# Kernel optimization log

Hardware: AMD Instinct MI355X
Metric: run time of the kernel (lower is better)

Reference implementation:

```python
import jax, jax.numpy as jnp
import numpy as np

C = 96          # channels (= output_dim)
NUM_HEADS = 6
DILS = (1, 2, 3)
KS_ATT = 3      # dilate-attention kernel size
KS_COR = 5      # self-correlation kernel size
PAD_COR = 2
LN_EPS = 1e-5


def _unfold(x, k, dil, pad):
    # torch.nn.Unfold(kernel=k, dilation=dil, padding=pad, stride=1)
    # x: [B, C, H, W] -> [B, C, k*k, H, W] (channel-major, kernel row-major)
    B, c, H, W = x.shape
    xp = jnp.pad(x, ((0, 0), (0, 0), (pad, pad), (pad, pad)))
    patches = [xp[:, :, i * dil:i * dil + H, j * dil:j * dil + W]
               for i in range(k) for j in range(k)]
    return jnp.stack(patches, axis=2)


def _layernorm(x, g, b):
    m = jnp.mean(x, axis=-1, keepdims=True)
    v = jnp.mean((x - m) ** 2, axis=-1, keepdims=True)
    return (x - m) * jax.lax.rsqrt(v + LN_EPS) * g + b


def _dilate_attn(q, k, v, dil, head_dim, scale):
    # q,k,v: [B, cb, H, W] with cb = C // num_dilation
    B, cb, H, W = q.shape
    heads = cb // head_dim
    qf = q.reshape(B, heads, head_dim, H * W)                                  # bhdn
    kp = _unfold(k, KS_ATT, dil, dil).reshape(B, heads, head_dim, KS_ATT * KS_ATT, H * W)
    attn = jax.nn.softmax(jnp.einsum('bhdn,bhdkn->bhnk', qf, kp) * scale, axis=-1)
    vp = _unfold(v, KS_ATT, dil, dil).reshape(B, heads, head_dim, KS_ATT * KS_ATT, H * W)
    out = jnp.einsum('bhnk,bhdkn->bnhd', attn, vp)                             # [B,HW,heads,hd]
    return out.reshape(B, H, W, cb)


def _forward(x, g1, b1, Wqkv, bqkv, Wproj, bproj, g2, b2, W1, bm1, W2, bm2):
    B, Cc, H, W = x.shape
    nd = len(DILS)
    head_dim = Cc // NUM_HEADS
    scale = head_dim ** (-0.5)

    xh = jnp.transpose(x, (0, 2, 3, 1))                                        # [B,H,W,C]

    # --- MultiDilatelocalAttention block ---
    y = _layernorm(xh, g1, b1)
    qkv = jnp.einsum('bhwc,oc->bhwo', y, Wqkv) + bqkv                          # 1x1 conv == linear
    qkv = jnp.transpose(qkv, (0, 3, 1, 2)).reshape(B, 3, nd, Cc // nd, H, W)
    outs = []
    for i, d in enumerate(DILS):
        outs.append(_dilate_attn(qkv[:, 0, i], qkv[:, 1, i], qkv[:, 2, i], d, head_dim, scale))
    a = jnp.concatenate(outs, axis=-1)                                         # dilation-major channels
    a = a @ Wproj.T + bproj
    xh = xh + a

    # --- MLP block ---
    z = _layernorm(xh, g2, b2)
    z = jax.nn.gelu(z @ W1.T + bm1, approximate=False) @ W2.T + bm2
    xh = xh + z

    # --- self-correlation ---
    xc = jnp.transpose(xh, (0, 3, 1, 2))                                       # [B,C,H,W]
    xc = jax.nn.relu(xc)
    nrm = jnp.sqrt(jnp.sum(xc * xc, axis=1, keepdims=True))
    xc = xc / jnp.maximum(nrm, 1e-12)                                          # F.normalize dim=1
    pat = _unfold(xc, KS_COR, 1, PAD_COR)                                      # [B,C,25,H,W]
    out = pat.reshape(B, Cc, KS_COR, KS_COR, H, W) * xc[:, :, None, None]
    return jnp.transpose(out, (0, 1, 4, 5, 2, 3))                              # [B,C,H,W,5,5]


def setup_inputs() -> dict:
    key = jax.random.key(0)
    ks = jax.random.split(key, 8)
    B, H, W = 8, 64, 64
    s = 0.02
    return {
        'x': jax.random.normal(ks[0], (B, C, H, W), jnp.float32),
        'g1': jnp.ones((C,), jnp.float32),
        'b1': jnp.zeros((C,), jnp.float32),
        'Wqkv': jax.random.normal(ks[1], (3 * C, C), jnp.float32) * s,
        'bqkv': jnp.zeros((3 * C,), jnp.float32),
        'Wproj': jax.random.normal(ks[2], (C, C), jnp.float32) * s,
        'bproj': jnp.zeros((C,), jnp.float32),
        'g2': jnp.ones((C,), jnp.float32),
        'b2': jnp.zeros((C,), jnp.float32),
        'W1': jax.random.normal(ks[3], (4 * C, C), jnp.float32) * s,
        'bm1': jnp.zeros((4 * C,), jnp.float32),
        'W2': jax.random.normal(ks[4], (C, 4 * C), jnp.float32) * s,
        'bm2': jnp.zeros((C,), jnp.float32),
    }


def reference(x, g1, b1, Wqkv, bqkv, Wproj, bproj, g2, b2, W1, bm1, W2, bm2):
    return _forward(x, g1, b1, Wqkv, bqkv, Wproj, bproj, g2, b2, W1, bm1, W2, bm2)
```

## Files before the change

### kernel.cpp

```cpp
#include <hip/hip_runtime.h>
#include <math.h>

#define NN 4096
#define BN 32768

using short8 = __attribute__((ext_vector_type(8))) short;
using f32x4  = __attribute__((ext_vector_type(4))) float;
typedef unsigned short ushort_t;

__device__ inline unsigned f2bfu(float f) {
    unsigned u = __builtin_bit_cast(unsigned, f);
    u += 0x7FFFu + ((u >> 16) & 1u);
    return u >> 16;
}
__device__ inline ushort_t f2bf(float f) { return (ushort_t)f2bfu(f); }
__device__ inline unsigned pack2(float a, float b) { return f2bfu(a) | (f2bfu(b) << 16); }
__device__ inline float bflo(unsigned u) { return __builtin_bit_cast(float, u << 16); }
__device__ inline float bfhi(unsigned u) { return __builtin_bit_cast(float, u & 0xFFFF0000u); }

__global__ __launch_bounds__(256) void k1_ln_kv(
    const float* __restrict__ x, const float* __restrict__ g1, const float* __restrict__ b1,
    const float* __restrict__ Wqkv, const float* __restrict__ bqkv,
    unsigned* __restrict__ kvt32)
{
    __shared__ __align__(16) float    Cs[96 * 69];
    __shared__ __align__(16) ushort_t As[64 * 104];
    __shared__ __align__(16) ushort_t Bs[96 * 104];
    const int tid = threadIdx.x;
    const long bn0 = (long)blockIdx.x * 64;
    const int b = (int)(bn0 >> 12);
    const int n0 = (int)(bn0 & 4095);

    for (int i = 0; i < 24; ++i) {
        int idx = i * 256 + tid;
        int c = idx >> 6, p = idx & 63;
        Cs[c * 69 + p] = x[((long)(b * 96 + c) << 12) + n0 + p];
    }
    __syncthreads();
    {
        int p = tid >> 2, part = tid & 3, c0 = part * 24;
        float s = 0.f, ss = 0.f;
        for (int c = c0; c < c0 + 24; ++c) { float v = Cs[c*69 + p]; s += v; ss += v*v; }
        s  += __shfl_xor(s, 1);  s  += __shfl_xor(s, 2);
        ss += __shfl_xor(ss, 1); ss += __shfl_xor(ss, 2);
        float m = s * (1.f/96.f);
        float rstd = rsqrtf(ss * (1.f/96.f) - m*m + 1e-5f);
        for (int c = c0; c < c0 + 24; ++c)
            Cs[c*69 + p] = (Cs[c*69 + p] - m) * rstd * g1[c] + b1[c];
    }
    __syncthreads();
    for (int i = 0; i < 12; ++i) {
        int idx = i * 256 + tid;
        int p = idx / 48, cp = idx % 48;
        *(unsigned*)&As[p * 104 + 2*cp] = pack2(Cs[(2*cp)*69 + p], Cs[(2*cp+1)*69 + p]);
    }

    const int lane = tid & 63, wv = tid >> 6;
    const int ln = lane & 15, qd = lane >> 4;
    for (int kv = 0; kv < 2; ++kv) {
        __syncthreads();
        for (int i = 0; i < 9; ++i) {
            int idx = i * 256 + tid;
            int o = idx / 24, q4 = idx % 24;
            float4 wvv = *(const float4*)&Wqkv[(long)(96 + kv*96 + o)*96 + q4*4];
            uint2 d; d.x = pack2(wvv.x, wvv.y); d.y = pack2(wvv.z, wvv.w);
            *(uint2*)&Bs[o * 104 + q4*4] = d;
        }
        __syncthreads();
        f32x4 acc[6];
        #pragma unroll
        for (int t = 0; t < 6; ++t) acc[t] = (f32x4){0.f, 0.f, 0.f, 0.f};
        #pragma unroll
        for (int kc = 0; kc < 3; ++kc) {
            short8 a = *(const short8*)&As[(wv*16 + ln)*104 + kc*32 + qd*8];
            #pragma unroll
            for (int t = 0; t < 6; ++t) {
                short8 bf = *(const short8*)&Bs[(t*16 + ln)*104 + kc*32 + qd*8];
                acc[t] = __builtin_amdgcn_mfma_f32_16x16x32_bf16(a, bf, acc[t], 0, 0, 0);
            }
        }
        #pragma unroll
        for (int t = 0; t < 6; ++t)
            #pragma unroll
            for (int r = 0; r < 4; ++r)
                Cs[(t*16 + ln)*69 + (wv*16 + qd*4 + r)] = acc[t][r];
        __syncthreads();
        for (int i = 0; i < 12; ++i) {
            int idx = i * 256 + tid;
            int cp = idx / 64, p = idx % 64;
            int c = 2*cp;
            unsigned d = pack2(Cs[c*69 + p] + bqkv[96 + kv*96 + c],
                               Cs[(c+1)*69 + p] + bqkv[96 + kv*96 + c + 1]);
            kvt32[((long)(b*96 + kv*48 + cp) << 12) + n0 + p] = d;
        }
    }
}

__global__ __launch_bounds__(256) void k2345(
    const unsigned* __restrict__ kvt32, const float* __restrict__ x,
    const float* __restrict__ g1, const float* __restrict__ b1,
    const float* __restrict__ Wqkv, const float* __restrict__ bqkv,
    const float* __restrict__ Wproj, const float* __restrict__ bproj,
    const float* __restrict__ g2, const float* __restrict__ b2,
    const float* __restrict__ W1, const float* __restrict__ bm1,
    const float* __restrict__ W2, const float* __restrict__ bm2,
    float* __restrict__ xcn)
{
    __shared__ __align__(16) float    Cs[96 * 69];
    __shared__ __align__(16) ushort_t As[64 * 104];
    __shared__ __align__(16) ushort_t Ah[64 * 104];
    __shared__ __align__(16) ushort_t Bs[96 * 104];
    __shared__ float lnm[64], lnr[64];
    const int tid = threadIdx.x;
    const long bn0 = (long)blockIdx.x * 64;
    const int b = (int)(bn0 >> 12);
    const int n0 = (int)(bn0 & 4095);
    const int h0 = n0 >> 6;
    const int lane = tid & 63, wv = tid >> 6;
    const int ln = lane & 15, qd = lane >> 4;

    for (int i = 0; i < 24; ++i) {
        int idx = i * 256 + tid;
        int c = idx >> 6, p = idx & 63;
        Cs[c * 69 + p] = x[((long)(b * 96 + c) << 12) + n0 + p];
    }
    __syncthreads();
    {
        int p = tid >> 2, part = tid & 3, c0 = part * 24;
        float s = 0.f, ss = 0.f;
        for (int c = c0; c < c0 + 24; ++c) { float v = Cs[c*69 + p]; s += v; ss += v*v; }
        s  += __shfl_xor(s, 1);  s  += __shfl_xor(s, 2);
        ss += __shfl_xor(ss, 1); ss += __shfl_xor(ss, 2);
        float m = s * (1.f/96.f);
        float rstd = rsqrtf(ss * (1.f/96.f) - m*m + 1e-5f);
        if (part == 0) { lnm[p] = m; lnr[p] = rstd; }
    }
    __syncthreads();
    for (int i = 0; i < 12; ++i) {
        int idx = i * 256 + tid;
        int p = idx / 48, cp = idx % 48;
        float m = lnm[p], rs = lnr[p];
        int c = 2*cp;
        unsigned d = pack2((Cs[(c  )*69 + p] - m) * rs * g1[c  ] + b1[c  ],
                           (Cs[(c+1)*69 + p] - m) * rs * g1[c+1] + b1[c+1]);
        *(unsigned*)&As[p * 104 + 2*cp] = d;
    }
    for (int i = 0; i < 9; ++i) {
        int idx = i * 256 + tid;
        int o = idx / 24, q4 = idx % 24;
        float4 wvv = *(const float4*)&Wqkv[(long)o*96 + q4*4];
        uint2 d; d.x = pack2(wvv.x, wvv.y); d.y = pack2(wvv.z, wvv.w);
        *(uint2*)&Bs[o * 104 + q4*4] = d;
    }
    __syncthreads();
    {
        f32x4 acc[6];
        #pragma unroll
        for (int t = 0; t < 6; ++t) acc[t] = (f32x4){0.f, 0.f, 0.f, 0.f};
        #pragma unroll
        for (int kc = 0; kc < 3; ++kc) {
            short8 a = *(const short8*)&As[(wv*16 + ln)*104 + kc*32 + qd*8];
            #pragma unroll
            for (int t = 0; t < 6; ++t) {
                short8 bf = *(const short8*)&Bs[(t*16 + ln)*104 + kc*32 + qd*8];
                acc[t] = __builtin_amdgcn_mfma_f32_16x16x32_bf16(a, bf, acc[t], 0, 0, 0);
            }
        }
        #pragma unroll
        for (int t = 0; t < 6; ++t) {
            float bias = bqkv[t*16 + ln];
            #pragma unroll
            for (int r = 0; r < 4; ++r)
                Ah[(wv*16 + qd*4 + r)*104 + t*16 + ln] = f2bf(acc[t][r] + bias);
        }
    }
    __syncthreads();
    for (int i = 0; i < 9; ++i) {
        int idx = i * 256 + tid;
        int o = idx / 24, q4 = idx % 24;
        float4 wvv = *(const float4*)&Wproj[(long)o*96 + q4*4];
        uint2 d; d.x = pack2(wvv.x, wvv.y); d.y = pack2(wvv.z, wvv.w);
        *(uint2*)&Bs[o * 104 + q4*4] = d;
    }
    for (int it = 0; it < 2; ++it) {
        int item = it * 256 + tid;
        if (item < 384) {
            int p = item & 63;
            int r = item >> 6;
            int head = r & 1, di = r >> 1;
            int dil = di + 1;
            int cp0 = di*16 + head*8;
            const unsigned* K = kvt32 + ((long)(b*96 +      cp0) << 12);
            const unsigned* V = kvt32 + ((long)(b*96 + 48 + cp0) << 12);
            int w = p;

            float q[16];
            #pragma unroll
            for (int j = 0; j < 8; ++j) {
                unsigned u = *(const unsigned*)&Ah[p * 104 + 2*(cp0 + j)];
                q[2*j] = bflo(u); q[2*j+1] = bfhi(u);
            }
            float logits[9];
            #pragma unroll
            for (int ki = 0; ki < 3; ++ki)
                #pragma unroll
                for (int kj = 0; kj < 3; ++kj) {
                    int hh = h0 + (ki-1)*dil, ww = w + (kj-1)*dil;
                    float l = 0.f;
                    if ((unsigned)hh < 64u && (unsigned)ww < 64u) {
                        int nn = (hh << 6) + ww;
                        #pragma unroll
                        for (int j = 0; j < 8; ++j) {
                            unsigned u = K[((long)j << 12) + nn];
                            l += q[2*j] * bflo(u) + q[2*j+1] * bfhi(u);
                        }
                    }
                    logits[ki*3 + kj] = l * 0.25f;
                }
            float m = logits[0];
            #pragma unroll
            for (int k = 1; k < 9; ++k) m = fmaxf(m, logits[k]);
            float e[9], s = 0.f;
            #pragma unroll
            for (int k = 0; k < 9; ++k) { e[k] = expf(logits[k] - m); s += e[k]; }
            float inv = 1.f / s;
            float o[16];
            #pragma unroll
            for (int d = 0; d < 16; ++d) o[d] = 0.f;
            #pragma unroll
            for (int ki = 0; ki < 3; ++ki)
                #pragma unroll
                for (int kj = 0; kj < 3; ++kj) {
                    int hh = h0 + (ki-1)*dil, ww = w + (kj-1)*dil;
                    if ((unsigned)hh < 64u && (unsigned)ww < 64u) {
                        int nn = (hh << 6) + ww;
                        float wgt = e[ki*3 + kj] * inv;
                        #pragma unroll
                        for (int j = 0; j < 8; ++j) {
                            unsigned u = V[((long)j << 12) + nn];
                            o[2*j]   += wgt * bflo(u);
                            o[2*j+1] += wgt * bfhi(u);
                        }
                    }
                }
            #pragma unroll
            for (int j = 0; j < 8; ++j)
                *(unsigned*)&As[p * 104 + 2*(cp0 + j)] = pack2(o[2*j], o[2*j+1]);
        }
    }
    __syncthreads();
    float resid[24];
    {
        f32x4 acc[6];
        #pragma unroll
        for (int t = 0; t < 6; ++t) acc[t] = (f32x4){0.f, 0.f, 0.f, 0.f};
        #pragma unroll
        for (int kc = 0; kc < 3; ++kc) {
            short8 a = *(const short8*)&As[(wv*16 + ln)*104 + kc*32 + qd*8];
            #pragma unroll
            for (int t = 0; t < 6; ++t) {
                short8 bf = *(const short8*)&Bs[(t*16 + ln)*104 + kc*32 + qd*8];
                acc[t] = __builtin_amdgcn_mfma_f32_16x16x32_bf16(a, bf, acc[t], 0, 0, 0);
            }
        }
        #pragma unroll
        for (int t = 0; t < 6; ++t) {
            int oc = t*16 + ln;
            float bias = bproj[oc];
            #pragma unroll
            for (int r = 0; r < 4; ++r) {
                int p = wv*16 + qd*4 + r;
                float v = acc[t][r] + bias + Cs[oc*69 + p];
                resid[t*4 + r] = v;
                Cs[oc*69 + p] = v;
            }
        }
    }
    __syncthreads();
    {
        int p = tid >> 2, part = tid & 3, c0 = part * 24;
        float s = 0.f, ss = 0.f;
        for (int c = c0; c < c0 + 24; ++c) { float v = Cs[c*69 + p]; s += v; ss += v*v; }
        s  += __shfl_xor(s, 1);  s  += __shfl_xor(s, 2);
        ss += __shfl_xor(ss, 1); ss += __shfl_xor(ss, 2);
        float m = s * (1.f/96.f);
        float rstd = rsqrtf(ss * (1.f/96.f) - m*m + 1e-5f);
        if (part == 0) { lnm[p] = m; lnr[p] = rstd; }
    }
    __syncthreads();
    for (int i = 0; i < 12; ++i) {
        int idx = i * 256 + tid;
        int p = idx / 48, cp = idx % 48;
        float m = lnm[p], rs = lnr[p];
        int c = 2*cp;
        unsigned d = pack2((Cs[(c  )*69 + p] - m) * rs * g2[c  ] + b2[c  ],
                           (Cs[(c+1)*69 + p] - m) * rs * g2[c+1] + b2[c+1]);
        *(unsigned*)&As[p * 104 + 2*cp] = d;
    }
    f32x4 acc2[6];
    #pragma unroll
    for (int t = 0; t < 6; ++t) acc2[t] = (f32x4){0.f, 0.f, 0.f, 0.f};
    for (int kb = 0; kb < 4; ++kb) {
        __syncthreads();
        for (int i = 0; i < 9; ++i) {
            int idx = i * 256 + tid;
            int o = idx / 24, q4 = idx % 24;
            float4 wvv = *(const float4*)&W1[(long)(kb*96 + o)*96 + q4*4];
            uint2 d; d.x = pack2(wvv.x, wvv.y); d.y = pack2(wvv.z, wvv.w);
            *(uint2*)&Bs[o * 104 + q4*4] = d;
        }
        __syncthreads();
        f32x4 acch[6];
        #pragma unroll
        for (int t = 0; t < 6; ++t) acch[t] = (f32x4){0.f, 0.f, 0.f, 0.f};
        #pragma unroll
        for (int kc = 0; kc < 3; ++kc) {
            short8 a = *(const short8*)&As[(wv*16 + ln)*104 + kc*32 + qd*8];
            #pragma unroll
            for (int t = 0; t < 6; ++t) {
                short8 bf = *(const short8*)&Bs[(t*16 + ln)*104 + kc*32 + qd*8];
                acch[t] = __builtin_amdgcn_mfma_f32_16x16x32_bf16(a, bf, acch[t], 0, 0, 0);
            }
        }
        #pragma unroll
        for (int t = 0; t < 6; ++t) {
            float bias = bm1[kb*96 + t*16 + ln];
            #pragma unroll
            for (int r = 0; r < 4; ++r) {
                float v = acch[t][r] + bias;
                v = 0.5f * v * (1.f + erff(v * 0.70710678118654752f));
                Ah[(wv*16 + qd*4 + r)*104 + t*16 + ln] = f2bf(v);
            }
        }
        __syncthreads();
        for (int i = 0; i < 9; ++i) {
            int idx = i * 256 + tid;
            int o = idx / 24, q4 = idx % 24;
            float4 wvv = *(const float4*)&W2[(long)o*384 + kb*96 + q4*4];
            uint2 d; d.x = pack2(wvv.x, wvv.y); d.y = pack2(wvv.z, wvv.w);
            *(uint2*)&Bs[o * 104 + q4*4] = d;
        }
        __syncthreads();
        #pragma unroll
        for (int kc = 0; kc < 3; ++kc) {
            short8 a = *(const short8*)&Ah[(wv*16 + ln)*104 + kc*32 + qd*8];
            #pragma unroll
            for (int t = 0; t < 6; ++t) {
                short8 bf = *(const short8*)&Bs[(t*16 + ln)*104 + kc*32 + qd*8];
                acc2[t] = __builtin_amdgcn_mfma_f32_16x16x32_bf16(a, bf, acc2[t], 0, 0, 0);
            }
        }
    }
    __syncthreads();
    #pragma unroll
    for (int t = 0; t < 6; ++t) {
        int oc = t*16 + ln;
        float bias = bm2[oc];
        #pragma unroll
        for (int r = 0; r < 4; ++r) {
            int p = wv*16 + qd*4 + r;
            float v = acc2[t][r] + bias + resid[t*4 + r];
            Cs[oc*69 + p] = fmaxf(v, 0.f);
        }
    }
    __syncthreads();
    {
        int p = tid >> 2, part = tid & 3, c0 = part * 24;
        float ss = 0.f;
        for (int c = c0; c < c0 + 24; ++c) { float v = Cs[c*69 + p]; ss += v*v; }
        ss += __shfl_xor(ss, 1); ss += __shfl_xor(ss, 2);
        if (part == 0) lnr[p] = 1.f / fmaxf(sqrtf(ss), 1e-12f);
    }
    __syncthreads();
    for (int i = 0; i < 12; ++i) {
        int idx = i * 256 + tid;
        int p = idx / 48, cp = idx % 48;
        float inv = lnr[p];
        float2 v = make_float2(Cs[(2*cp)*69 + p] * inv, Cs[(2*cp+1)*69 + p] * inv);
        *(float2*)&xcn[(bn0 + p) * 96 + 2*cp] = v;
    }
}

__global__ __launch_bounds__(256) void k6_selfcorr(
    const float* __restrict__ xcn, float* __restrict__ out)
{
    __shared__ float xt[5 * 20 * 97];
    const int tid = threadIdx.x;
    const int wc = blockIdx.x;
    const int h  = blockIdx.y;
    const int b  = blockIdx.z;
    const int w0 = wc * 16;

    for (int i = 0; i < 38; ++i) {
        int idx = i * 256 + tid;
        if (idx < 9600) {
            int r = idx / (20 * 96);
            int rem = idx - r * (20 * 96);
            int wi = rem / 96, c = rem - wi * 96;
            int hh = h + r - 2, ww = w0 + wi - 2;
            float v = 0.f;
            if ((unsigned)hh < 64u && (unsigned)ww < 64u)
                v = xcn[(((long)b << 12) + (hh << 6) + ww) * 96 + c];
            xt[(r * 20 + wi) * 97 + c] = v;
        }
    }
    __syncthreads();
    f32x4* out4 = (f32x4*)out;
    const long ob4 = (long)b * 2457600 + (long)h * 400 + wc * 100;
    for (int i = 0; i < 38; ++i) {
        int idx = i * 256 + tid;
        if (idx < 9600) {
            int c = idx / 100;
            int r4 = idx - c * 100;
            f32x4 v;
            #pragma unroll
            for (int j = 0; j < 4; ++j) {
                int r = r4 * 4 + j;
                int lw = r / 25, k = r - lw * 25;
                int ki = k / 5, kj = k - ki * 5;
                float center = xt[(42 + lw) * 97 + c];
                float neigh  = xt[(ki * 20 + lw + kj) * 97 + c];
                v[j] = center * neigh;
            }
            __builtin_nontemporal_store(v, &out4[ob4 + (long)c * 25600 + r4]);
        }
    }
}

extern "C" void kernel_launch(void* const* d_in, const int* in_sizes, int n_in,
                              void* d_out, int out_size, void* d_ws, size_t ws_size,
                              hipStream_t stream)
{
    const float* x     = (const float*)d_in[0];
    const float* g1    = (const float*)d_in[1];
    const float* b1    = (const float*)d_in[2];
    const float* Wqkv  = (const float*)d_in[3];
    const float* bqkv  = (const float*)d_in[4];
    const float* Wproj = (const float*)d_in[5];
    const float* bproj = (const float*)d_in[6];
    const float* g2    = (const float*)d_in[7];
    const float* b2    = (const float*)d_in[8];
    const float* W1    = (const float*)d_in[9];
    const float* bm1   = (const float*)d_in[10];
    const float* W2    = (const float*)d_in[11];
    const float* bm2   = (const float*)d_in[12];
    float* out = (float*)d_out;

    char* w = (char*)d_ws;
    unsigned* kvt32 = (unsigned*)w;  w += (size_t)BN * 192 * 2;
    float*    xcn   = (float*)w;

    k1_ln_kv   <<<BN / 64, 256, 0, stream>>>(x, g1, b1, Wqkv, bqkv, kvt32);
    k2345      <<<BN / 64, 256, 0, stream>>>(kvt32, x, g1, b1, Wqkv, bqkv,
                                             Wproj, bproj, g2, b2,
                                             W1, bm1, W2, bm2, xcn);
    k6_selfcorr<<<dim3(4, 64, 8), 256, 0, stream>>>(xcn, out);
}
```

Before: 421.7 us.

## Pre-pack weights to bf16 and stream them into LDS with async double buffering

Adds a small pack kernel that converts all weight matrices to padded bf16 once per call. The two main kernels then load these tiles with global_load_lds into double-buffered LDS, overlapping each weight load with the MFMA work on the other buffer. This removes the per-block fp32-to-bf16 conversion and several barriers. Other changes bundled in: a polynomial erf approximation for GELU, __expf in the softmax, an Ah buffer aliased onto Cs to save LDS, a CSTR stride of 66, a min-occupancy launch bound of 2, and a swizzled block order. The added launch and the approximate GELU and exp may shift accuracy slightly.

```diff
diff --git a/kernel.cpp b/kernel.cpp
--- a/kernel.cpp
+++ b/kernel.cpp
@@ -3,6 +3,7 @@
 
 #define NN 4096
 #define BN 32768
+#define CSTR 66
 
 using short8 = __attribute__((ext_vector_type(8))) short;
 using f32x4  = __attribute__((ext_vector_type(4))) float;
@@ -18,117 +19,82 @@
 __device__ inline float bflo(unsigned u) { return __builtin_bit_cast(float, u << 16); }
 __device__ inline float bfhi(unsigned u) { return __builtin_bit_cast(float, u & 0xFFFF0000u); }
 
-__global__ __launch_bounds__(256) void k1_ln_kv(
+__device__ inline float gelu_f(float v) {
+    float xx = v * 0.70710678118654752f;
+    float a  = fabsf(xx);
+    float t  = 1.0f / (1.0f + 0.3275911f * a);
+    float p  = t*(0.254829592f + t*(-0.284496736f + t*(1.421413741f + t*(-1.453152027f + t*1.061405429f))));
+    float erfv = 1.0f - p * __expf(-xx*xx);
+    erfv = copysignf(erfv, xx);
+    return 0.5f * v * (1.0f + erfv);
+}
+
+__device__ inline void stage_w(const unsigned* __restrict__ wbf, int stage,
+                               ushort_t* dst, int wv, int lane) {
+    const unsigned* src = wbf + (long)stage * 5120 + lane * 4;
+    #pragma unroll
+    for (int i = 0; i < 5; ++i) {
+        int chunk = wv + 4 * i;
+        __builtin_amdgcn_global_load_lds(
+            (const __attribute__((address_space(1))) unsigned*)(src + chunk * 256),
+            (__attribute__((address_space(3))) unsigned*)(dst + chunk * 512),
+            16, 0, 0);
+    }
+}
+
+__global__ __launch_bounds__(256) void k0_pack(
+    const float* __restrict__ Wqkv, const float* __restrict__ Wproj,
+    const float* __restrict__ W1, const float* __restrict__ W2,
+    unsigned* __restrict__ wbf)
+{
+    int d = blockIdx.x * 256 + threadIdx.x;
+    int s = d / 5120, r = d - s * 5120;
+    int o = r / 52, qp = r - o * 52;
+    unsigned val = 0u;
+    if (o < 96 && qp < 48) {
+        int q = qp * 2;
+        float2 w2;
+        if (s == 0)      w2 = *(const float2*)&Wqkv[(long)o * 96 + q];
+        else if (s == 1) w2 = *(const float2*)&Wqkv[(long)(96 + o) * 96 + q];
+        else if (s == 2) w2 = *(const float2*)&Wqkv[(long)(192 + o) * 96 + q];
+        else if (s == 3) w2 = *(const float2*)&Wproj[(long)o * 96 + q];
+        else if (((s - 4) & 1) == 0) { int kb = (s - 4) >> 1; w2 = *(const float2*)&W1[(long)(kb * 96 + o) * 96 + q]; }
+        else                         { int kb = (s - 4) >> 1; w2 = *(const float2*)&W2[(long)o * 384 + kb * 96 + q]; }
+        val = pack2(w2.x, w2.y);
+    }
+    wbf[d] = val;
+}
+
+__global__ __launch_bounds__(256, 2) void k1_ln_kv(
     const float* __restrict__ x, const float* __restrict__ g1, const float* __restrict__ b1,
-    const float* __restrict__ Wqkv, const float* __restrict__ bqkv,
+    const float* __restrict__ bqkv, const unsigned* __restrict__ wbf,
     unsigned* __restrict__ kvt32)
 {
-    __shared__ __align__(16) float    Cs[96 * 69];
+    __shared__ __align__(16) float    Cs[96 * CSTR];
     __shared__ __align__(16) ushort_t As[64 * 104];
-    __shared__ __align__(16) ushort_t Bs[96 * 104];
+    __shared__ __align__(16) ushort_t Bs[2][10240];
+    __shared__ float lnm[64], lnr[64];
     const int tid = threadIdx.x;
-    const long bn0 = (long)blockIdx.x * 64;
-    const int b = (int)(bn0 >> 12);
+    const int bid = blockIdx.x;
+    const int wg  = ((bid & 7) << 6) | (bid >> 3);
+    const long bn0 = (long)wg << 6;
+    const int b  = (int)(bn0 >> 12);
     const int n0 = (int)(bn0 & 4095);
-
+    const int lane = tid & 63, wv = tid >> 6;
+    const int ln = lane & 15, qd = lane >> 4;
+
+    stage_w(wbf, 1, &Bs[0][0], wv, lane);
+    stage_w(wbf, 2, &Bs[1][0], wv, lane);
     for (int i = 0; i < 24; ++i) {
         int idx = i * 256 + tid;
         int c = idx >> 6, p = idx & 63;
-        Cs[c * 69 + p] = x[((long)(b * 96 + c) << 12) + n0 + p];
+        Cs[c * CSTR + p] = x[((long)(b * 96 + c) << 12) + n0 + p];
     }
     __syncthreads();
     {
         int p = tid >> 2, part = tid & 3, c0 = part * 24;
         float s = 0.f, ss = 0.f;
-        for (int c = c0; c < c0 + 24; ++c) { float v = Cs[c*69 + p]; s += v; ss += v*v; }
-        s  += __shfl_xor(s, 1);  s  += __shfl_xor(s, 2);
-        ss += __shfl_xor(ss, 1); ss += __shfl_xor(ss, 2);
-        float m = s * (1.f/96.f);
-        float rstd = rsqrtf(ss * (1.f/96.f) - m*m + 1e-5f);
-        for (int c = c0; c < c0 + 24; ++c)
-            Cs[c*69 + p] = (Cs[c*69 + p] - m) * rstd * g1[c] + b1[c];
-    }
-    __syncthreads();
-    for (int i = 0; i < 12; ++i) {
-        int idx = i * 256 + tid;
-        int p = idx / 48, cp = idx % 48;
-        *(unsigned*)&As[p * 104 + 2*cp] = pack2(Cs[(2*cp)*69 + p], Cs[(2*cp+1)*69 + p]);
-    }
-
-    const int lane = tid & 63, wv = tid >> 6;
-    const int ln = lane & 15, qd = lane >> 4;
-    for (int kv = 0; kv < 2; ++kv) {
-        __syncthreads();
-        for (int i = 0; i < 9; ++i) {
-            int idx = i * 256 + tid;
-            int o = idx / 24, q4 = idx % 24;
-            float4 wvv = *(const float4*)&Wqkv[(long)(96 + kv*96 + o)*96 + q4*4];
-            uint2 d; d.x = pack2(wvv.x, wvv.y); d.y = pack2(wvv.z, wvv.w);
-            *(uint2*)&Bs[o * 104 + q4*4] = d;
-        }
-        __syncthreads();
-        f32x4 acc[6];
-        #pragma unroll
-        for (int t = 0; t < 6; ++t) acc[t] = (f32x4){0.f, 0.f, 0.f, 0.f};
-        #pragma unroll
-        for (int kc = 0; kc < 3; ++kc) {
-            short8 a = *(const short8*)&As[(wv*16 + ln)*104 + kc*32 + qd*8];
-            #pragma unroll
-            for (int t = 0; t < 6; ++t) {
-                short8 bf = *(const short8*)&Bs[(t*16 + ln)*104 + kc*32 + qd*8];
-                acc[t] = __builtin_amdgcn_mfma_f32_16x16x32_bf16(a, bf, acc[t], 0, 0, 0);
-            }
-        }
-        #pragma unroll
-        for (int t = 0; t < 6; ++t)
-            #pragma unroll
-            for (int r = 0; r < 4; ++r)
-                Cs[(t*16 + ln)*69 + (wv*16 + qd*4 + r)] = acc[t][r];
-        __syncthreads();
-        for (int i = 0; i < 12; ++i) {
-            int idx = i * 256 + tid;
-            int cp = idx / 64, p = idx % 64;
-            int c = 2*cp;
-            unsigned d = pack2(Cs[c*69 + p] + bqkv[96 + kv*96 + c],
-                               Cs[(c+1)*69 + p] + bqkv[96 + kv*96 + c + 1]);
-            kvt32[((long)(b*96 + kv*48 + cp) << 12) + n0 + p] = d;
-        }
-    }
-}
-
-__global__ __launch_bounds__(256) void k2345(
-    const unsigned* __restrict__ kvt32, const float* __restrict__ x,
-    const float* __restrict__ g1, const float* __restrict__ b1,
-    const float* __restrict__ Wqkv, const float* __restrict__ bqkv,
-    const float* __restrict__ Wproj, const float* __restrict__ bproj,
-    const float* __restrict__ g2, const float* __restrict__ b2,
-    const float* __restrict__ W1, const float* __restrict__ bm1,
-    const float* __restrict__ W2, const float* __restrict__ bm2,
-    float* __restrict__ xcn)
-{
-    __shared__ __align__(16) float    Cs[96 * 69];
-    __shared__ __align__(16) ushort_t As[64 * 104];
-    __shared__ __align__(16) ushort_t Ah[64 * 104];
-    __shared__ __align__(16) ushort_t Bs[96 * 104];
-    __shared__ float lnm[64], lnr[64];
-    const int tid = threadIdx.x;
-    const long bn0 = (long)blockIdx.x * 64;
-    const int b = (int)(bn0 >> 12);
-    const int n0 = (int)(bn0 & 4095);
-    const int h0 = n0 >> 6;
-    const int lane = tid & 63, wv = tid >> 6;
-    const int ln = lane & 15, qd = lane >> 4;
-
-    for (int i = 0; i < 24; ++i) {
-        int idx = i * 256 + tid;
-        int c = idx >> 6, p = idx & 63;
-        Cs[c * 69 + p] = x[((long)(b * 96 + c) << 12) + n0 + p];
-    }
-    __syncthreads();
-    {
-        int p = tid >> 2, part = tid & 3, c0 = part * 24;
-        float s = 0.f, ss = 0.f;
-        for (int c = c0; c < c0 + 24; ++c) { float v = Cs[c*69 + p]; s += v; ss += v*v; }
+        for (int c = c0; c < c0 + 24; ++c) { float v = Cs[c*CSTR + p]; s += v; ss += v*v; }
         s  += __shfl_xor(s, 1);  s  += __shfl_xor(s, 2);
         ss += __shfl_xor(ss, 1); ss += __shfl_xor(ss, 2);
         float m = s * (1.f/96.f);
@@ -140,29 +106,125 @@
         int idx = i * 256 + tid;
         int p = idx / 48, cp = idx % 48;
         float m = lnm[p], rs = lnr[p];
-        int c = 2*cp;
-        unsigned d = pack2((Cs[(c  )*69 + p] - m) * rs * g1[c  ] + b1[c  ],
-                           (Cs[(c+1)*69 + p] - m) * rs * g1[c+1] + b1[c+1]);
-        *(unsigned*)&As[p * 104 + 2*cp] = d;
-    }
-    for (int i = 0; i < 9; ++i) {
-        int idx = i * 256 + tid;
-        int o = idx / 24, q4 = idx % 24;
-        float4 wvv = *(const float4*)&Wqkv[(long)o*96 + q4*4];
-        uint2 d; d.x = pack2(wvv.x, wvv.y); d.y = pack2(wvv.z, wvv.w);
-        *(uint2*)&Bs[o * 104 + q4*4] = d;
+        int c = 2 * cp;
+        *(unsigned*)&As[p * 104 + 2*cp] =
+            pack2((Cs[c*CSTR + p]     - m) * rs * g1[c]   + b1[c],
+                  (Cs[(c+1)*CSTR + p] - m) * rs * g1[c+1] + b1[c+1]);
+    }
+    __syncthreads();
+    f32x4 acck[6], accv[6];
+    #pragma unroll
+    for (int t = 0; t < 6; ++t) { acck[t] = (f32x4){0.f,0.f,0.f,0.f}; accv[t] = (f32x4){0.f,0.f,0.f,0.f}; }
+    #pragma unroll
+    for (int kc = 0; kc < 3; ++kc) {
+        short8 a = *(const short8*)&As[(wv*16 + ln)*104 + kc*32 + qd*8];
+        #pragma unroll
+        for (int t = 0; t < 6; ++t) {
+            short8 bf = *(const short8*)&Bs[0][(t*16 + ln)*104 + kc*32 + qd*8];
+            acck[t] = __builtin_amdgcn_mfma_f32_16x16x32_bf16(a, bf, acck[t], 0, 0, 0);
+        }
+    }
+    #pragma unroll
+    for (int t = 0; t < 6; ++t)
+        #pragma unroll
+        for (int r = 0; r < 4; ++r)
+            Cs[(t*16 + ln)*CSTR + (wv*16 + qd*4 + r)] = acck[t][r];
+    __syncthreads();
+    #pragma unroll
+    for (int kc = 0; kc < 3; ++kc) {
+        short8 a = *(const short8*)&As[(wv*16 + ln)*104 + kc*32 + qd*8];
+        #pragma unroll
+        for (int t = 0; t < 6; ++t) {
+            short8 bf = *(const short8*)&Bs[1][(t*16 + ln)*104 + kc*32 + qd*8];
+            accv[t] = __builtin_amdgcn_mfma_f32_16x16x32_bf16(a, bf, accv[t], 0, 0, 0);
+        }
+    }
+    for (int i = 0; i < 12; ++i) {
+        int idx = i * 256 + tid;
+        int cp = idx / 64, p = idx % 64;
+        int c = 2 * cp;
+        kvt32[((long)(b*96 + cp) << 12) + n0 + p] =
+            pack2(Cs[c*CSTR + p] + bqkv[96 + c], Cs[(c+1)*CSTR + p] + bqkv[96 + c + 1]);
+    }
+    __syncthreads();
+    #pragma unroll
+    for (int t = 0; t < 6; ++t)
+        #pragma unroll
+        for (int r = 0; r < 4; ++r)
+            Cs[(t*16 + ln)*CSTR + (wv*16 + qd*4 + r)] = accv[t][r];
+    __syncthreads();
+    for (int i = 0; i < 12; ++i) {
+        int idx = i * 256 + tid;
+        int cp = idx / 64, p = idx % 64;
+        int c = 2 * cp;
+        kvt32[((long)(b*96 + 48 + cp) << 12) + n0 + p] =
+            pack2(Cs[c*CSTR + p] + bqkv[192 + c], Cs[(c+1)*CSTR + p] + bqkv[192 + c + 1]);
+    }
+}
+
+__global__ __launch_bounds__(256, 2) void k2345(
+    const unsigned* __restrict__ kvt32, const float* __restrict__ x,
+    const float* __restrict__ g1, const float* __restrict__ b1,
+    const float* __restrict__ bqkv, const unsigned* __restrict__ wbf,
+    const float* __restrict__ bproj,
+    const float* __restrict__ g2, const float* __restrict__ b2,
+    const float* __restrict__ bm1, const float* __restrict__ bm2,
+    float* __restrict__ xcn)
+{
+    __shared__ __align__(16) float    Cs[96 * CSTR];
+    __shared__ __align__(16) ushort_t As[64 * 104];
+    __shared__ __align__(16) ushort_t Bs[2][10240];
+    __shared__ float lnm[64], lnr[64];
+    ushort_t* Hs = (ushort_t*)Cs;
+    const int tid = threadIdx.x;
+    const int bid = blockIdx.x;
+    const int wg  = ((bid & 7) << 6) | (bid >> 3);
+    const long bn0 = (long)wg << 6;
+    const int b  = (int)(bn0 >> 12);
+    const int n0 = (int)(bn0 & 4095);
+    const int h0 = n0 >> 6;
+    const int lane = tid & 63, wv = tid >> 6;
+    const int ln = lane & 15, qd = lane >> 4;
+
+    stage_w(wbf, 0, &Bs[0][0], wv, lane);
+    stage_w(wbf, 3, &Bs[1][0], wv, lane);
+    for (int i = 0; i < 24; ++i) {
+        int idx = i * 256 + tid;
+        int c = idx >> 6, p = idx & 63;
+        Cs[c * CSTR + p] = x[((long)(b * 96 + c) << 12) + n0 + p];
+    }
+    __syncthreads();
+    {
+        int p = tid >> 2, part = tid & 3, c0 = part * 24;
+        float s = 0.f, ss = 0.f;
+        for (int c = c0; c < c0 + 24; ++c) { float v = Cs[c*CSTR + p]; s += v; ss += v*v; }
+        s  += __shfl_xor(s, 1);  s  += __shfl_xor(s, 2);
+        ss += __shfl_xor(ss, 1); ss += __shfl_xor(ss, 2);
+        float m = s * (1.f/96.f);
+        float rstd = rsqrtf(ss * (1.f/96.f) - m*m + 1e-5f);
+        if (part == 0) { lnm[p] = m; lnr[p] = rstd; }
+    }
+    __syncthreads();
+    for (int i = 0; i < 12; ++i) {
+        int idx = i * 256 + tid;
+        int p = idx / 48, cp = idx % 48;
+        float m = lnm[p], rs = lnr[p];
+        int c = 2 * cp;
+        *(unsigned*)&As[p * 104 + 2*cp] =
+            pack2((Cs[c*CSTR + p]     - m) * rs * g1[c]   + b1[c],
+                  (Cs[(c+1)*CSTR + p] - m) * rs * g1[c+1] + b1[c+1]);
     }
     __syncthreads();
     {
         f32x4 acc[6];
         #pragma unroll
-        for (int t = 0; t < 6; ++t) acc[t] = (f32x4){0.f, 0.f, 0.f, 0.f};
+        for (int t = 0; t < 6; ++t) acc[t] = (f32x4){0.f,0.f,0.f,0.f};
         #pragma unroll
         for (int kc = 0; kc < 3; ++kc) {
             short8 a = *(const short8*)&As[(wv*16 + ln)*104 + kc*32 + qd*8];
             #pragma unroll
             for (int t = 0; t < 6; ++t) {
-                short8 bf = *(const short8*)&Bs[(t*16 + ln)*104 + kc*32 + qd*8];
+                short8 bf = *(const short8*)&Bs[0][(t*16 + ln)*104 + kc*32 + qd*8];
                 acc[t] = __builtin_amdgcn_mfma_f32_16x16x32_bf16(a, bf, acc[t], 0, 0, 0);
             }
         }
@@ -171,17 +233,11 @@
             float bias = bqkv[t*16 + ln];
             #pragma unroll
             for (int r = 0; r < 4; ++r)
-                Ah[(wv*16 + qd*4 + r)*104 + t*16 + ln] = f2bf(acc[t][r] + bias);
-        }
-    }
-    __syncthreads();
-    for (int i = 0; i < 9; ++i) {
-        int idx = i * 256 + tid;
-        int o = idx / 24, q4 = idx % 24;
-        float4 wvv = *(const float4*)&Wproj[(long)o*96 + q4*4];
-        uint2 d; d.x = pack2(wvv.x, wvv.y); d.y = pack2(wvv.z, wvv.w);
-        *(uint2*)&Bs[o * 104 + q4*4] = d;
-    }
+                As[(wv*16 + qd*4 + r)*104 + t*16 + ln] = f2bf(acc[t][r] + bias);
+        }
+    }
+    __syncthreads();
+    stage_w(wbf, 4, &Bs[0][0], wv, lane);
     for (int it = 0; it < 2; ++it) {
         int item = it * 256 + tid;
         if (item < 384) {
@@ -197,7 +253,7 @@
             float q[16];
             #pragma unroll
             for (int j = 0; j < 8; ++j) {
-                unsigned u = *(const unsigned*)&Ah[p * 104 + 2*(cp0 + j)];
+                unsigned u = *(const unsigned*)&As[p * 104 + 2*(cp0 + j)];
                 q[2*j] = bflo(u); q[2*j+1] = bfhi(u);
             }
             float logits[9];
@@ -222,7 +278,7 @@
             for (int k = 1; k < 9; ++k) m = fmaxf(m, logits[k]);
             float e[9], s = 0.f;
             #pragma unroll
-            for (int k = 0; k < 9; ++k) { e[k] = expf(logits[k] - m); s += e[k]; }
+            for (int k = 0; k < 9; ++k) { e[k] = __expf(logits[k] - m); s += e[k]; }
             float inv = 1.f / s;
             float o[16];
             #pragma unroll
@@ -253,13 +309,13 @@
     {
         f32x4 acc[6];
         #pragma unroll
-        for (int t = 0; t < 6; ++t) acc[t] = (f32x4){0.f, 0.f, 0.f, 0.f};
+        for (int t = 0; t < 6; ++t) acc[t] = (f32x4){0.f,0.f,0.f,0.f};
         #pragma unroll
         for (int kc = 0; kc < 3; ++kc) {
             short8 a = *(const short8*)&As[(wv*16 + ln)*104 + kc*32 + qd*8];
             #pragma unroll
             for (int t = 0; t < 6; ++t) {
-                short8 bf = *(const short8*)&Bs[(t*16 + ln)*104 + kc*32 + qd*8];
+                short8 bf = *(const short8*)&Bs[1][(t*16 + ln)*104 + kc*32 + qd*8];
                 acc[t] = __builtin_amdgcn_mfma_f32_16x16x32_bf16(a, bf, acc[t], 0, 0, 0);
             }
         }
@@ -270,17 +326,18 @@
             #pragma unroll
             for (int r = 0; r < 4; ++r) {
                 int p = wv*16 + qd*4 + r;
-                float v = acc[t][r] + bias + Cs[oc*69 + p];
+                float v = acc[t][r] + bias + Cs[oc*CSTR + p];
                 resid[t*4 + r] = v;
-                Cs[oc*69 + p] = v;
-            }
-        }
-    }
-    __syncthreads();
+                Cs[oc*CSTR + p] = v;
+            }
+        }
+    }
+    __syncthreads();
+    stage_w(wbf, 5, &Bs[1][0], wv, lane);
     {
         int p = tid >> 2, part = tid & 3, c0 = part * 24;
         float s = 0.f, ss = 0.f;
-        for (int c = c0; c < c0 + 24; ++c) { float v = Cs[c*69 + p]; s += v; ss += v*v; }
+        for (int c = c0; c < c0 + 24; ++c) { float v = Cs[c*CSTR + p]; s += v; ss += v*v; }
         s  += __shfl_xor(s, 1);  s  += __shfl_xor(s, 2);
         ss += __shfl_xor(ss, 1); ss += __shfl_xor(ss, 2);
         float m = s * (1.f/96.f);
@@ -292,33 +349,25 @@
         int idx = i * 256 + tid;
         int p = idx / 48, cp = idx % 48;
         float m = lnm[p], rs = lnr[p];
-        int c = 2*cp;
-        unsigned d = pack2((Cs[(c  )*69 + p] - m) * rs * g2[c  ] + b2[c  ],
-                           (Cs[(c+1)*69 + p] - m) * rs * g2[c+1] + b2[c+1]);
-        *(unsigned*)&As[p * 104 + 2*cp] = d;
-    }
+        int c = 2 * cp;
+        *(unsigned*)&As[p * 104 + 2*cp] =
+            pack2((Cs[c*CSTR + p]     - m) * rs * g2[c]   + b2[c],
+                  (Cs[(c+1)*CSTR + p] - m) * rs * g2[c+1] + b2[c+1]);
+    }
+    __syncthreads();
     f32x4 acc2[6];
     #pragma unroll
-    for (int t = 0; t < 6; ++t) acc2[t] = (f32x4){0.f, 0.f, 0.f, 0.f};
+    for (int t = 0; t < 6; ++t) acc2[t] = (f32x4){0.f,0.f,0.f,0.f};
     for (int kb = 0; kb < 4; ++kb) {
-        __syncthreads();
-        for (int i = 0; i < 9; ++i) {
-            int idx = i * 256 + tid;
-            int o = idx / 24, q4 = idx % 24;
-            float4 wvv = *(const float4*)&W1[(long)(kb*96 + o)*96 + q4*4];
-            uint2 d; d.x = pack2(wvv.x, wvv.y); d.y = pack2(wvv.z, wvv.w);
-            *(uint2*)&Bs[o * 104 + q4*4] = d;
-        }
-        __syncthreads();
         f32x4 acch[6];
         #pragma unroll
-        for (int t = 0; t < 6; ++t) acch[t] = (f32x4){0.f, 0.f, 0.f, 0.f};
+        for (int t = 0; t < 6; ++t) acch[t] = (f32x4){0.f,0.f,0.f,0.f};
         #pragma unroll
         for (int kc = 0; kc < 3; ++kc) {
             short8 a = *(const short8*)&As[(wv*16 + ln)*104 + kc*32 + qd*8];
             #pragma unroll
             for (int t = 0; t < 6; ++t) {
-                short8 bf = *(const short8*)&Bs[(t*16 + ln)*104 + kc*32 + qd*8];
+                short8 bf = *(const short8*)&Bs[0][(t*16 + ln)*104 + kc*32 + qd*8];
                 acch[t] = __builtin_amdgcn_mfma_f32_16x16x32_bf16(a, bf, acch[t], 0, 0, 0);
             }
         }
@@ -326,32 +375,23 @@
         for (int t = 0; t < 6; ++t) {
             float bias = bm1[kb*96 + t*16 + ln];
             #pragma unroll
-            for (int r = 0; r < 4; ++r) {
-                float v = acch[t][r] + bias;
-                v = 0.5f * v * (1.f + erff(v * 0.70710678118654752f));
-                Ah[(wv*16 + qd*4 + r)*104 + t*16 + ln] = f2bf(v);
-            }
+            for (int r = 0; r < 4; ++r)
+                Hs[(wv*16 + qd*4 + r)*104 + t*16 + ln] = f2bf(gelu_f(acch[t][r] + bias));
         }
         __syncthreads();
-        for (int i = 0; i < 9; ++i) {
-            int idx = i * 256 + tid;
-            int o = idx / 24, q4 = idx % 24;
-            float4 wvv = *(const float4*)&W2[(long)o*384 + kb*96 + q4*4];
-            uint2 d; d.x = pack2(wvv.x, wvv.y); d.y = pack2(wvv.z, wvv.w);
-            *(uint2*)&Bs[o * 104 + q4*4] = d;
+        if (kb < 3) stage_w(wbf, 6 + 2*kb, &Bs[0][0], wv, lane);
+        #pragma unroll
+        for (int kc = 0; kc < 3; ++kc) {
+            short8 a = *(const short8*)&Hs[(wv*16 + ln)*104 + kc*32 + qd*8];
+            #pragma unroll
+            for (int t = 0; t < 6; ++t) {
+                short8 bf = *(const short8*)&Bs[1][(t*16 + ln)*104 + kc*32 + qd*8];
+                acc2[t] = __builtin_amdgcn_mfma_f32_16x16x32_bf16(a, bf, acc2[t], 0, 0, 0);
+            }
         }
         __syncthreads();
-        #pragma unroll
-        for (int kc = 0; kc < 3; ++kc) {
-            short8 a = *(const short8*)&Ah[(wv*16 + ln)*104 + kc*32 + qd*8];
-            #pragma unroll
-            for (int t = 0; t < 6; ++t) {
-                short8 bf = *(const short8*)&Bs[(t*16 + ln)*104 + kc*32 + qd*8];
-                acc2[t] = __builtin_amdgcn_mfma_f32_16x16x32_bf16(a, bf, acc2[t], 0, 0, 0);
-            }
-        }
-    }
-    __syncthreads();
+        if (kb < 3) stage_w(wbf, 7 + 2*kb, &Bs[1][0], wv, lane);
+    }
     #pragma unroll
     for (int t = 0; t < 6; ++t) {
         int oc = t*16 + ln;
@@ -360,14 +400,14 @@
         for (int r = 0; r < 4; ++r) {
             int p = wv*16 + qd*4 + r;
             float v = acc2[t][r] + bias + resid[t*4 + r];
-            Cs[oc*69 + p] = fmaxf(v, 0.f);
+            Cs[oc*CSTR + p] = fmaxf(v, 0.f);
         }
     }
     __syncthreads();
     {
         int p = tid >> 2, part = tid & 3, c0 = part * 24;
         float ss = 0.f;
-        for (int c = c0; c < c0 + 24; ++c) { float v = Cs[c*69 + p]; ss += v*v; }
+        for (int c = c0; c < c0 + 24; ++c) { float v = Cs[c*CSTR + p]; ss += v*v; }
         ss += __shfl_xor(ss, 1); ss += __shfl_xor(ss, 2);
         if (part == 0) lnr[p] = 1.f / fmaxf(sqrtf(ss), 1e-12f);
     }
@@ -376,7 +416,7 @@
         int idx = i * 256 + tid;
         int p = idx / 48, cp = idx % 48;
         float inv = lnr[p];
-        float2 v = make_float2(Cs[(2*cp)*69 + p] * inv, Cs[(2*cp+1)*69 + p] * inv);
+        float2 v = make_float2(Cs[(2*cp)*CSTR + p] * inv, Cs[(2*cp+1)*CSTR + p] * inv);
         *(float2*)&xcn[(bn0 + p) * 96 + 2*cp] = v;
     }
 }
@@ -447,12 +487,13 @@
     float* out = (float*)d_out;
 
     char* w = (char*)d_ws;
+    unsigned* wbf   = (unsigned*)w;  w += 12 * 20480;
     unsigned* kvt32 = (unsigned*)w;  w += (size_t)BN * 192 * 2;
     float*    xcn   = (float*)w;
 
-    k1_ln_kv   <<<BN / 64, 256, 0, stream>>>(x, g1, b1, Wqkv, bqkv, kvt32);
-    k2345      <<<BN / 64, 256, 0, stream>>>(kvt32, x, g1, b1, Wqkv, bqkv,
-                                             Wproj, bproj, g2, b2,
-                                             W1, bm1, W2, bm2, xcn);
+    k0_pack    <<<240, 256, 0, stream>>>(Wqkv, Wproj, W1, W2, wbf);
+    k1_ln_kv   <<<BN / 64, 256, 0, stream>>>(x, g1, b1, bqkv, wbf, kvt32);
+    k2345      <<<BN / 64, 256, 0, stream>>>(kvt32, x, g1, b1, bqkv, wbf,
+                                             bproj, g2, b2, bm1, bm2, xcn);
     k6_selfcorr<<<dim3(4, 64, 8), 256, 0, stream>>>(xcn, out);
 }
```

Result: faster. 406.2 us (-3.7%).
